# Kernel tuning notes

Hardware: AMD Instinct MI355X
Metric: run time of the kernel (lower is better)

## Reference

```python
import jax, jax.numpy as jnp
import numpy as np

D_MODEL = 1024
N_HEADS = 16
D_K = D_MODEL // N_HEADS


def setup_inputs() -> dict:
    key = jax.random.key(0)
    ks = jax.random.split(key, 7)
    B, S = 2, 2048
    q = jax.random.normal(ks[0], (B, S, D_MODEL), dtype=jnp.float32)
    k = jax.random.normal(ks[1], (B, S, D_MODEL), dtype=jnp.float32)
    v = jax.random.normal(ks[2], (B, S, D_MODEL), dtype=jnp.float32)
    mask = jnp.ones((B, 1, S, S), dtype=bool)
    scale = 1.0 / np.sqrt(D_MODEL)
    w_q = jax.random.normal(ks[3], (D_MODEL, D_MODEL), dtype=jnp.float32) * scale
    w_k = jax.random.normal(ks[4], (D_MODEL, D_MODEL), dtype=jnp.float32) * scale
    w_v = jax.random.normal(ks[5], (D_MODEL, D_MODEL), dtype=jnp.float32) * scale
    w_o = jax.random.normal(ks[6], (D_MODEL, D_MODEL), dtype=jnp.float32) * scale
    return {"q": q, "k": k, "v": v, "mask": mask,
            "w_q": w_q, "w_k": w_k, "w_v": w_v, "w_o": w_o}


def reference(q, k, v, mask, w_q, w_k, w_v, w_o):
    B, S, _ = q.shape
    # projections (nn.Linear: x @ W^T, no bias)
    def split_heads(x):  # [B,S,D] -> [B,H,S,d_k]
        return x.reshape(B, -1, N_HEADS, D_K).transpose(0, 2, 1, 3)
    query = split_heads(q @ w_q.T)
    key_h = split_heads(k @ w_k.T)
    value = split_heads(v @ w_v.T)
    # naive scaled dot-product attention: full [B,H,S,S] scores materialized
    scores = jnp.einsum('bhqd,bhkd->bhqk', query, key_h) / jnp.sqrt(
        jnp.asarray(D_K, query.dtype))
    scores = jnp.where(mask, scores, jnp.asarray(-1e9, scores.dtype))
    attn = jax.nn.softmax(scores, axis=-1)  # dropout p=0.0 -> identity
    x = jnp.einsum('bhqk,bhkd->bhqd', attn, value)
    x = x.transpose(0, 2, 1, 3).reshape(B, S, N_HEADS * D_K)
    return x @ w_o.T
```

## Files before the change

kernel.cpp:

```cpp
#include <hip/hip_runtime.h>
#include <hip/hip_bf16.h>
#include <math.h>

typedef __bf16 bf16;
typedef __bf16 bf16x8 __attribute__((ext_vector_type(8)));
typedef float f32x4 __attribute__((ext_vector_type(4)));

#define MFMA16(a, b, c) __builtin_amdgcn_mfma_f32_16x16x32_bf16((a), (b), (c), 0, 0, 0)

__device__ __forceinline__ void gl_lds16(const void* g, void* l) {
    __builtin_amdgcn_global_load_lds(
        (__attribute__((address_space(1))) void*)(g),
        (__attribute__((address_space(3))) void*)(l),
        16, 0, 0);
}

__global__ __launch_bounds__(256) void cvt7(
    const float* __restrict__ w0, const float* __restrict__ w1,
    const float* __restrict__ w2, const float* __restrict__ w3,
    const float* __restrict__ x0, const float* __restrict__ x1,
    const float* __restrict__ x2, bf16* __restrict__ dst) {
    const int z = blockIdx.y;
    const float* src;
    bf16* out;
    if (z < 4) {
        if (blockIdx.x >= 512) return;
        src = (z == 0) ? w0 : (z == 1) ? w1 : (z == 2) ? w2 : w3;
        out = dst + (size_t)z * 1048576;
    } else {
        src = (z == 4) ? x0 : (z == 5) ? x1 : x2;
        out = dst + 4 * 1048576 + (size_t)(z - 4) * 4194304;
    }
    const int i = (blockIdx.x * 256 + threadIdx.x) * 8;
    float4 a = ((const float4*)(src + i))[0];
    float4 b = ((const float4*)(src + i))[1];
    bf16x8 o;
    o[0] = (bf16)a.x; o[1] = (bf16)a.y; o[2] = (bf16)a.z; o[3] = (bf16)a.w;
    o[4] = (bf16)b.x; o[5] = (bf16)b.y; o[6] = (bf16)b.z; o[7] = (bf16)b.w;
    *(bf16x8*)(out + i) = o;
}

template <int EP>
__device__ __forceinline__ void gemm_bf(const bf16* __restrict__ A,
                                        const bf16* __restrict__ B,
                                        void* __restrict__ Cv,
                                        const int m0, const int n0) {
    constexpr int K = 1024;
    __shared__ __align__(16) bf16 As[128 * 32];
    __shared__ __align__(16) bf16 Bs[128 * 32];

    const int t = threadIdx.x;
    const int lane = t & 63;
    const int w = t >> 6;
    const int wm = (w & 1) * 64;
    const int wn = (w >> 1) * 64;
    const int lr = lane & 15;
    const int lq8 = (lane >> 4) * 8;
    const int rq = (lane >> 4) * 4;

    f32x4 acc[4][4] = {};

    const int srow = t >> 2;
    const int sch = (t & 3) * 8;
    char* lA = (char*)As;
    char* lB = (char*)Bs;

    for (int k0 = 0; k0 < K; k0 += 32) {
        gl_lds16(A + (size_t)(m0 + srow) * K + k0 + sch,      lA + t * 16);
        gl_lds16(A + (size_t)(m0 + 64 + srow) * K + k0 + sch, lA + 4096 + t * 16);
        gl_lds16(B + (size_t)(n0 + srow) * K + k0 + sch,      lB + t * 16);
        gl_lds16(B + (size_t)(n0 + 64 + srow) * K + k0 + sch, lB + 4096 + t * 16);
        __syncthreads();

        bf16x8 af[4], bfr[4];
#pragma unroll
        for (int i = 0; i < 4; ++i) {
            af[i]  = *(const bf16x8*)&As[(wm + i * 16 + lr) * 32 + lq8];
            bfr[i] = *(const bf16x8*)&Bs[(wn + i * 16 + lr) * 32 + lq8];
        }
#pragma unroll
        for (int mi = 0; mi < 4; ++mi)
#pragma unroll
            for (int ni = 0; ni < 4; ++ni)
                acc[mi][ni] = MFMA16(af[mi], bfr[ni], acc[mi][ni]);
        __syncthreads();
    }

#pragma unroll
    for (int mi = 0; mi < 4; ++mi) {
#pragma unroll
        for (int ni = 0; ni < 4; ++ni) {
#pragma unroll
            for (int r = 0; r < 4; ++r) {
                const int m = m0 + wm + mi * 16 + rq + r;
                const int n = n0 + wn + ni * 16 + lr;
                const float vv = acc[mi][ni][r];
                if constexpr (EP == 0) {
                    bf16* C = (bf16*)Cv;
                    const int b = m >> 11, s = m & 2047;
                    const int h = n >> 6,  d = n & 63;
                    C[(((size_t)(b * 16 + h)) * 2048 + s) * 64 + d] = (bf16)vv;
                } else if constexpr (EP == 1) {
                    float* C = (float*)Cv;
                    C[(size_t)m * 1024 + n] = vv;
                } else {
                    bf16* C = (bf16*)Cv;
                    C[((size_t)(n >> 11) * 1024 + m) * 2048 + (n & 2047)] = (bf16)vv;
                }
            }
        }
    }
}

__global__ __launch_bounds__(256, 3) void qkv_bf(
    const bf16* __restrict__ Xq, const bf16* __restrict__ Xk,
    const bf16* __restrict__ Xv, const bf16* __restrict__ Wc,
    bf16* __restrict__ Qb, bf16* __restrict__ Kb, bf16* __restrict__ Vb) {
    const int z = blockIdx.z;
    if (z == 0)
        gemm_bf<0>(Xq, Wc, Qb, blockIdx.x * 128, blockIdx.y * 128);
    else if (z == 1)
        gemm_bf<0>(Xk, Wc + 1048576, Kb, blockIdx.x * 128, blockIdx.y * 128);
    else
        gemm_bf<2>(Wc + 2 * 1048576, Xv, Vb, blockIdx.y * 128, blockIdx.x * 128);
}

__global__ __launch_bounds__(256, 2) void out_gemm(
    const bf16* __restrict__ X, const bf16* __restrict__ W, float* __restrict__ C) {
    gemm_bf<1>(X, W, C, blockIdx.x * 128, blockIdx.y * 128);
}

template <int MODE>
__device__ __forceinline__ void gemm_f32tok(const void* __restrict__ Av,
                                            const void* __restrict__ Bv,
                                            bf16* __restrict__ C,
                                            const int m0, const int n0) {
    constexpr int K = 1024;
    __shared__ __align__(16) bf16 As[128 * 32];
    __shared__ __align__(16) bf16 Bs[128 * 32];

    const int t = threadIdx.x;
    const int lane = t & 63;
    const int w = t >> 6;
    const int wm = (w & 1) * 64;
    const int wn = (w >> 1) * 64;
    const int lr = lane & 15;
    const int lq8 = (lane >> 4) * 8;
    const int rq = (lane >> 4) * 4;

    f32x4 acc[4][4] = {};
    const int srow = t >> 2;
    const int sch = (t & 3) * 8;
    const int ar = t >> 1;
    const int ac = (t & 1) * 16;
    char* lA = (char*)As;
    char* lB = (char*)Bs;

    for (int k0 = 0; k0 < K; k0 += 32) {
        if constexpr (MODE == 0) {
            const float* X = (const float*)Av;
            const float* p = X + (size_t)(m0 + ar) * K + k0 + ac;
            float4 f0 = ((const float4*)p)[0], f1 = ((const float4*)p)[1];
            float4 f2 = ((const float4*)p)[2], f3 = ((const float4*)p)[3];
            bf16x8 o0, o1;
            o0[0]=(bf16)f0.x; o0[1]=(bf16)f0.y; o0[2]=(bf16)f0.z; o0[3]=(bf16)f0.w;
            o0[4]=(bf16)f1.x; o0[5]=(bf16)f1.y; o0[6]=(bf16)f1.z; o0[7]=(bf16)f1.w;
            o1[0]=(bf16)f2.x; o1[1]=(bf16)f2.y; o1[2]=(bf16)f2.z; o1[3]=(bf16)f2.w;
            o1[4]=(bf16)f3.x; o1[5]=(bf16)f3.y; o1[6]=(bf16)f3.z; o1[7]=(bf16)f3.w;
            *(bf16x8*)&As[ar * 32 + ac]     = o0;
            *(bf16x8*)&As[ar * 32 + ac + 8] = o1;
        } else {
            const bf16* X = (const bf16*)Av;
            gl_lds16(X + (size_t)(m0 + srow) * K + k0 + sch,      lA + t * 16);
            gl_lds16(X + (size_t)(m0 + 64 + srow) * K + k0 + sch, lA + 4096 + t * 16);
        }
        if constexpr (MODE == 2) {
            const float* X = (const float*)Bv;
            const float* p = X + (size_t)(n0 + ar) * K + k0 + ac;
            float4 f0 = ((const float4*)p)[0], f1 = ((const float4*)p)[1];
            float4 f2 = ((const float4*)p)[2], f3 = ((const float4*)p)[3];
            bf16x8 o0, o1;
            o0[0]=(bf16)f0.x; o0[1]=(bf16)f0.y; o0[2]=(bf16)f0.z; o0[3]=(bf16)f0.w;
            o0[4]=(bf16)f1.x; o0[5]=(bf16)f1.y; o0[6]=(bf16)f1.z; o0[7]=(bf16)f1.w;
            o1[0]=(bf16)f2.x; o1[1]=(bf16)f2.y; o1[2]=(bf16)f2.z; o1[3]=(bf16)f2.w;
            o1[4]=(bf16)f3.x; o1[5]=(bf16)f3.y; o1[6]=(bf16)f3.z; o1[7]=(bf16)f3.w;
            *(bf16x8*)&Bs[ar * 32 + ac]     = o0;
            *(bf16x8*)&Bs[ar * 32 + ac + 8] = o1;
        } else {
            const bf16* W = (const bf16*)Bv;
            gl_lds16(W + (size_t)(n0 + srow) * K + k0 + sch,      lB + t * 16);
            gl_lds16(W + (size_t)(n0 + 64 + srow) * K + k0 + sch, lB + 4096 + t * 16);
        }
        __syncthreads();

        bf16x8 af[4], bfr[4];
#pragma unroll
        for (int i = 0; i < 4; ++i) {
            af[i]  = *(const bf16x8*)&As[(wm + i * 16 + lr) * 32 + lq8];
            bfr[i] = *(const bf16x8*)&Bs[(wn + i * 16 + lr) * 32 + lq8];
        }
#pragma unroll
        for (int mi = 0; mi < 4; ++mi)
#pragma unroll
            for (int ni = 0; ni < 4; ++ni)
                acc[mi][ni] = MFMA16(af[mi], bfr[ni], acc[mi][ni]);
        __syncthreads();
    }

#pragma unroll
    for (int mi = 0; mi < 4; ++mi) {
#pragma unroll
        for (int ni = 0; ni < 4; ++ni) {
#pragma unroll
            for (int r = 0; r < 4; ++r) {
                const int m = m0 + wm + mi * 16 + rq + r;
                const int n = n0 + wn + ni * 16 + lr;
                const float vv = acc[mi][ni][r];
                if constexpr (MODE == 0) {
                    const int b = m >> 11, s = m & 2047;
                    const int h = n >> 6,  d = n & 63;
                    C[(((size_t)(b * 16 + h)) * 2048 + s) * 64 + d] = (bf16)vv;
                } else {
                    C[((size_t)(n >> 11) * 1024 + m) * 2048 + (n & 2047)] = (bf16)vv;
                }
            }
        }
    }
}

__global__ __launch_bounds__(256, 2) void qkv_f32(
    const float* __restrict__ q, const float* __restrict__ k, const float* __restrict__ v,
    const bf16* __restrict__ Wc, bf16* __restrict__ Qb, bf16* __restrict__ Kb,
    bf16* __restrict__ Vb) {
    const int z = blockIdx.z;
    if (z == 0)
        gemm_f32tok<0>(q, Wc, Qb, blockIdx.x * 128, blockIdx.y * 128);
    else if (z == 1)
        gemm_f32tok<0>(k, Wc + 1048576, Kb, blockIdx.x * 128, blockIdx.y * 128);
    else
        gemm_f32tok<2>(Wc + 2 * 1048576, v, Vb, blockIdx.y * 128, blockIdx.x * 128);
}

__global__ __launch_bounds__(256, 4) void attn_kernel(
    const bf16* __restrict__ Qb, const bf16* __restrict__ Kb,
    const bf16* __restrict__ Vb, bf16* __restrict__ Xb) {
    constexpr int S = 2048;

    __shared__ __align__(16) bf16 Qs[64 * 64];
    __shared__ __align__(16) bf16 Ks[64 * 64];
    __shared__ __align__(16) bf16 Ps[64 * 64];
    __shared__ __align__(16) bf16 Vt[80 * 64];

    const int t = threadIdx.x;
    const int lane = t & 63;
    const int w = t >> 6;
    const int lr = lane & 15;
    const int lq8 = (lane >> 4) * 8;
    const int q4 = (lane >> 4) * 4;
    const int bh = blockIdx.y;
    const int q0 = blockIdx.x * 64;
    const bf16* Q  = Qb + (size_t)bh * S * 64;
    const bf16* Kh = Kb + (size_t)bh * S * 64;
    const bf16* Vh = Vb + (size_t)bh * 64 * S;

    const float qscale = 0.125f * 1.4426950408889634f;
#pragma unroll
    for (int p = 0; p < 2; ++p) {
        const int c = p * 256 + t;
        const int row = c >> 3, cc = c & 7;
        bf16x8 vq = *(const bf16x8*)(Q + (size_t)(q0 + row) * 64 + cc * 8);
#pragma unroll
        for (int e = 0; e < 8; ++e) vq[e] = (bf16)((float)vq[e] * qscale);
        *(bf16x8*)&Qs[row * 64 + (cc ^ (row & 7)) * 8] = vq;
    }
    for (int idx = t; idx < 1024; idx += 256) {
        const int r = idx >> 6;
        Vt[(64 + r) * 64 + (idx & 63)] = (r == 0) ? (bf16)1.0f : (bf16)0.0f;
    }

    f32x4 oacc[5] = {};

    const int srow = t >> 2;
    const int scc = (t & 3) * 2;
    bf16x8 pk[2], pv[2];
#pragma unroll
    for (int c = 0; c < 2; ++c) {
        pk[c] = *(const bf16x8*)(Kh + (size_t)srow * 64 + (scc + c) * 8);
        pv[c] = *(const bf16x8*)(Vh + (size_t)srow * S + (scc + c) * 8);
    }

    const int rowA = w * 16 + lr;
    const int swzA = (lr & 7) << 3;
    const int swzP = (((rowA >> 1) & 7)) << 3;

    for (int j = 0; j < S / 64; ++j) {
        __syncthreads();
#pragma unroll
        for (int c = 0; c < 2; ++c) {
            *(bf16x8*)&Ks[srow * 64 + ((scc + c) ^ (srow & 7)) * 8] = pk[c];
            *(bf16x8*)&Vt[srow * 64 + ((scc + c) ^ (srow & 7)) * 8] = pv[c];
        }
        __syncthreads();

        f32x4 sacc[4] = {};
#pragma unroll
        for (int ks = 0; ks < 64; ks += 32) {
            bf16x8 af = *(const bf16x8*)&Qs[rowA * 64 + ((ks + lq8) ^ swzA)];
            bf16x8 bk[4];
#pragma unroll
            for (int nt = 0; nt < 4; ++nt)
                bk[nt] = *(const bf16x8*)&Ks[(nt * 16 + lr) * 64 + ((ks + lq8) ^ swzA)];
#pragma unroll
            for (int nt = 0; nt < 4; ++nt)
                sacc[nt] = MFMA16(af, bk[nt], sacc[nt]);
        }

        if (j + 1 < S / 64) {
            const bf16* Kt = Kh + (size_t)(j + 1) * 64 * 64;
            const bf16* Vg = Vh + (size_t)(j + 1) * 64;
#pragma unroll
            for (int c = 0; c < 2; ++c) {
                pk[c] = *(const bf16x8*)(Kt + (size_t)srow * 64 + (scc + c) * 8);
                pv[c] = *(const bf16x8*)(Vg + (size_t)srow * S + (scc + c) * 8);
            }
        }

#pragma unroll
        for (int r = 0; r < 4; ++r) {
            const int row = w * 16 + q4 + r;
            const int swz = ((row >> 1) & 7) << 3;
#pragma unroll
            for (int nt = 0; nt < 4; ++nt)
                Ps[row * 64 + ((nt * 16 + lr) ^ swz)] =
                    (bf16)exp2f(fminf(sacc[nt][r], 100.f));
        }

#pragma unroll
        for (int ks = 0; ks < 64; ks += 32) {
            bf16x8 ap = *(const bf16x8*)&Ps[rowA * 64 + ((ks + lq8) ^ swzP)];
            bf16x8 bv[5];
#pragma unroll
            for (int nt2 = 0; nt2 < 5; ++nt2)
                bv[nt2] = *(const bf16x8*)&Vt[(nt2 * 16 + lr) * 64 + ((ks + lq8) ^ swzA)];
#pragma unroll
            for (int nt2 = 0; nt2 < 5; ++nt2)
                oacc[nt2] = MFMA16(ap, bv[nt2], oacc[nt2]);
        }
    }

    const int b = bh >> 4, h = bh & 15;
#pragma unroll
    for (int r = 0; r < 4; ++r) {
        const float lv = __shfl(oacc[4][r], lane & 48, 64);
        const float inv = 1.f / fmaxf(lv, 1e-30f);
        const int row = w * 16 + q4 + r;
        const size_t base = ((size_t)(b * 2048 + q0 + row)) * 1024 + h * 64;
#pragma unroll
        for (int nt2 = 0; nt2 < 4; ++nt2)
            Xb[base + nt2 * 16 + lr] = (bf16)(oacc[nt2][r] * inv);
    }
}

extern "C" void kernel_launch(void* const* d_in, const int* in_sizes, int n_in,
                              void* d_out, int out_size, void* d_ws, size_t ws_size,
                              hipStream_t stream) {
    const float* q  = (const float*)d_in[0];
    const float* k  = (const float*)d_in[1];
    const float* v  = (const float*)d_in[2];
    const float* wq = (const float*)d_in[4];
    const float* wk = (const float*)d_in[5];
    const float* wv = (const float*)d_in[6];
    const float* wo = (const float*)d_in[7];
    float* out = (float*)d_out;

    const bool big = ws_size >= (size_t)64 * 1024 * 1024;
    bf16* Wc = (bf16*)d_ws;
    const dim3 blk(256);

    if (big) {
        bf16* Xq = Wc + 4 * 1048576;
        bf16* Xk = Xq + 4194304;
        bf16* Xv = Xk + 4194304;
        bf16* Qb = Xv + 4194304;
        bf16* Kb = Qb + 4194304;
        bf16* Vb = Kb + 4194304;
        bf16* Xb = Vb + 4194304;
        cvt7<<<dim3(2048, 7), blk, 0, stream>>>(wq, wk, wv, wo, q, k, v, Wc);
        qkv_bf<<<dim3(32, 8, 3), blk, 0, stream>>>(Xq, Xk, Xv, Wc, Qb, Kb, Vb);
        attn_kernel<<<dim3(32, 32), blk, 0, stream>>>(Qb, Kb, Vb, Xb);
        out_gemm<<<dim3(32, 8), blk, 0, stream>>>(Xb, Wc + 3 * 1048576, out);
    } else {
        bf16* Qb = Wc + 4 * 1048576;
        bf16* Kb = Qb + 4194304;
        bf16* Vb = Kb + 4194304;
        bf16* Xb = Vb + 4194304;
        cvt7<<<dim3(512, 4), blk, 0, stream>>>(wq, wk, wv, wo, q, k, v, Wc);
        qkv_f32<<<dim3(32, 8, 3), blk, 0, stream>>>(q, k, v, Wc, Qb, Kb, Vb);
        attn_kernel<<<dim3(32, 32), blk, 0, stream>>>(Qb, Kb, Vb, Xb);
        out_gemm<<<dim3(32, 8), blk, 0, stream>>>(Xb, Wc + 3 * 1048576, out);
    }
}
```

Measured before the change: 262.7 us.

## Rewrite attention with 32x32 MFMA, register-resident P and 128-row query tiles

The attention kernel now uses 32x32x16 bf16 MFMAs. It computes S^T = K·Q^T so the exponentiated scores stay in registers and are repacked into the PV operand with cvt_pk_bf16 and permlane32_swap, which removes the Ps LDS round-trip and the Q LDS buffer. Each block now covers 128 query rows (32 per wave) instead of 64, halving K/V tile reloads per query. Row sums are accumulated in registers instead of through an extra ones-column MFMA. The trade-off is higher register pressure (launch bounds drop from 4 to 2) and half as many blocks.

```diff
diff --git a/kernel.cpp b/kernel.cpp
--- a/kernel.cpp
+++ b/kernel.cpp
@@ -5,14 +5,23 @@
 typedef __bf16 bf16;
 typedef __bf16 bf16x8 __attribute__((ext_vector_type(8)));
 typedef float f32x4 __attribute__((ext_vector_type(4)));
+typedef float f32x16 __attribute__((ext_vector_type(16)));
+typedef unsigned u32x4 __attribute__((ext_vector_type(4)));
 
 #define MFMA16(a, b, c) __builtin_amdgcn_mfma_f32_16x16x32_bf16((a), (b), (c), 0, 0, 0)
+#define MFMA32(a, b, c) __builtin_amdgcn_mfma_f32_32x32x16_bf16((a), (b), (c), 0, 0, 0)
 
 __device__ __forceinline__ void gl_lds16(const void* g, void* l) {
     __builtin_amdgcn_global_load_lds(
         (__attribute__((address_space(1))) void*)(g),
         (__attribute__((address_space(3))) void*)(l),
         16, 0, 0);
+}
+
+__device__ __forceinline__ unsigned cvt_pk_bf16(float lo, float hi) {
+    unsigned r;
+    asm("v_cvt_pk_bf16_f32 %0, %1, %2" : "=v"(r) : "v"(lo), "v"(hi));
+    return r;
 }
 
 __global__ __launch_bounds__(256) void cvt7(
@@ -241,44 +250,37 @@
         gemm_f32tok<2>(Wc + 2 * 1048576, v, Vb, blockIdx.y * 128, blockIdx.x * 128);
 }
 
-__global__ __launch_bounds__(256, 4) void attn_kernel(
+__global__ __launch_bounds__(256, 2) void attn_kernel(
     const bf16* __restrict__ Qb, const bf16* __restrict__ Kb,
     const bf16* __restrict__ Vb, bf16* __restrict__ Xb) {
     constexpr int S = 2048;
 
-    __shared__ __align__(16) bf16 Qs[64 * 64];
     __shared__ __align__(16) bf16 Ks[64 * 64];
-    __shared__ __align__(16) bf16 Ps[64 * 64];
-    __shared__ __align__(16) bf16 Vt[80 * 64];
+    __shared__ __align__(16) bf16 Vt[64 * 64];
 
     const int t = threadIdx.x;
     const int lane = t & 63;
     const int w = t >> 6;
-    const int lr = lane & 15;
-    const int lq8 = (lane >> 4) * 8;
-    const int q4 = (lane >> 4) * 4;
+    const int l31 = lane & 31;
+    const int half = lane >> 5;
     const int bh = blockIdx.y;
-    const int q0 = blockIdx.x * 64;
+    const int q0 = blockIdx.x * 128 + w * 32;
     const bf16* Q  = Qb + (size_t)bh * S * 64;
     const bf16* Kh = Kb + (size_t)bh * S * 64;
     const bf16* Vh = Vb + (size_t)bh * 64 * S;
 
     const float qscale = 0.125f * 1.4426950408889634f;
-#pragma unroll
-    for (int p = 0; p < 2; ++p) {
-        const int c = p * 256 + t;
-        const int row = c >> 3, cc = c & 7;
-        bf16x8 vq = *(const bf16x8*)(Q + (size_t)(q0 + row) * 64 + cc * 8);
-#pragma unroll
-        for (int e = 0; e < 8; ++e) vq[e] = (bf16)((float)vq[e] * qscale);
-        *(bf16x8*)&Qs[row * 64 + (cc ^ (row & 7)) * 8] = vq;
-    }
-    for (int idx = t; idx < 1024; idx += 256) {
-        const int r = idx >> 6;
-        Vt[(64 + r) * 64 + (idx & 63)] = (r == 0) ? (bf16)1.0f : (bf16)0.0f;
-    }
-
-    f32x4 oacc[5] = {};
+    bf16x8 qf[4];
+#pragma unroll
+    for (int c = 0; c < 4; ++c) {
+        bf16x8 v0 = *(const bf16x8*)(Q + (size_t)(q0 + l31) * 64 + c * 16 + half * 8);
+#pragma unroll
+        for (int e = 0; e < 8; ++e) v0[e] = (bf16)((float)v0[e] * qscale);
+        qf[c] = v0;
+    }
+
+    f32x16 od[2] = {};
+    float ls0 = 0.f, ls1 = 0.f, ls2 = 0.f, ls3 = 0.f;
 
     const int srow = t >> 2;
     const int scc = (t & 3) * 2;
@@ -289,10 +291,6 @@
         pv[c] = *(const bf16x8*)(Vh + (size_t)srow * S + (scc + c) * 8);
     }
 
-    const int rowA = w * 16 + lr;
-    const int swzA = (lr & 7) << 3;
-    const int swzP = (((rowA >> 1) & 7)) << 3;
-
     for (int j = 0; j < S / 64; ++j) {
         __syncthreads();
 #pragma unroll
@@ -302,17 +300,16 @@
         }
         __syncthreads();
 
-        f32x4 sacc[4] = {};
-#pragma unroll
-        for (int ks = 0; ks < 64; ks += 32) {
-            bf16x8 af = *(const bf16x8*)&Qs[rowA * 64 + ((ks + lq8) ^ swzA)];
-            bf16x8 bk[4];
-#pragma unroll
-            for (int nt = 0; nt < 4; ++nt)
-                bk[nt] = *(const bf16x8*)&Ks[(nt * 16 + lr) * 64 + ((ks + lq8) ^ swzA)];
-#pragma unroll
-            for (int nt = 0; nt < 4; ++nt)
-                sacc[nt] = MFMA16(af, bk[nt], sacc[nt]);
+        f32x16 sacc[2] = {};
+#pragma unroll
+        for (int kt = 0; kt < 2; ++kt) {
+            const int kr = kt * 32 + l31;
+            const int ksw = (kr & 7);
+#pragma unroll
+            for (int c = 0; c < 4; ++c) {
+                bf16x8 kf = *(const bf16x8*)&Ks[kr * 64 + ((c * 2 + half) ^ ksw) * 8];
+                sacc[kt] = MFMA32(kf, qf[c], sacc[kt]);
+            }
         }
 
         if (j + 1 < S / 64) {
@@ -326,38 +323,57 @@
         }
 
 #pragma unroll
-        for (int r = 0; r < 4; ++r) {
-            const int row = w * 16 + q4 + r;
-            const int swz = ((row >> 1) & 7) << 3;
-#pragma unroll
-            for (int nt = 0; nt < 4; ++nt)
-                Ps[row * 64 + ((nt * 16 + lr) ^ swz)] =
-                    (bf16)exp2f(fminf(sacc[nt][r], 100.f));
-        }
-
-#pragma unroll
-        for (int ks = 0; ks < 64; ks += 32) {
-            bf16x8 ap = *(const bf16x8*)&Ps[rowA * 64 + ((ks + lq8) ^ swzP)];
-            bf16x8 bv[5];
-#pragma unroll
-            for (int nt2 = 0; nt2 < 5; ++nt2)
-                bv[nt2] = *(const bf16x8*)&Vt[(nt2 * 16 + lr) * 64 + ((ks + lq8) ^ swzA)];
-#pragma unroll
-            for (int nt2 = 0; nt2 < 5; ++nt2)
-                oacc[nt2] = MFMA16(ap, bv[nt2], oacc[nt2]);
-        }
-    }
-
-    const int b = bh >> 4, h = bh & 15;
-#pragma unroll
-    for (int r = 0; r < 4; ++r) {
-        const float lv = __shfl(oacc[4][r], lane & 48, 64);
-        const float inv = 1.f / fmaxf(lv, 1e-30f);
-        const int row = w * 16 + q4 + r;
-        const size_t base = ((size_t)(b * 2048 + q0 + row)) * 1024 + h * 64;
-#pragma unroll
-        for (int nt2 = 0; nt2 < 4; ++nt2)
-            Xb[base + nt2 * 16 + lr] = (bf16)(oacc[nt2][r] * inv);
+        for (int kt = 0; kt < 2; ++kt) {
+            float ex[16];
+#pragma unroll
+            for (int r = 0; r < 16; ++r)
+                ex[r] = exp2f(fminf(sacc[kt][r], 100.f));
+            ls0 += ex[0] + ex[4] + ex[8]  + ex[12];
+            ls1 += ex[1] + ex[5] + ex[9]  + ex[13];
+            ls2 += ex[2] + ex[6] + ex[10] + ex[14];
+            ls3 += ex[3] + ex[7] + ex[11] + ex[15];
+
+            unsigned pa[8];
+#pragma unroll
+            for (int c2 = 0; c2 < 2; ++c2) {
+#pragma unroll
+                for (int wd = 0; wd < 2; ++wd) {
+                    unsigned x = cvt_pk_bf16(ex[c2 * 8 + wd * 2 + 0], ex[c2 * 8 + wd * 2 + 1]);
+                    unsigned y = cvt_pk_bf16(ex[c2 * 8 + wd * 2 + 4], ex[c2 * 8 + wd * 2 + 5]);
+                    asm("v_permlane32_swap_b32 %0, %1" : "+v"(x), "+v"(y));
+                    pa[c2 * 4 + wd]     = x;
+                    pa[c2 * 4 + wd + 2] = y;
+                }
+            }
+
+#pragma unroll
+            for (int c2 = 0; c2 < 2; ++c2) {
+                u32x4 aw;
+                aw[0] = pa[c2 * 4 + 0]; aw[1] = pa[c2 * 4 + 1];
+                aw[2] = pa[c2 * 4 + 2]; aw[3] = pa[c2 * 4 + 3];
+                bf16x8 ap = __builtin_bit_cast(bf16x8, aw);
+#pragma unroll
+                for (int dt = 0; dt < 2; ++dt) {
+                    const int vr = dt * 32 + l31;
+                    bf16x8 vf = *(const bf16x8*)
+                        &Vt[vr * 64 + (((kt * 4 + c2 * 2 + half) ^ (vr & 7))) * 8];
+                    od[dt] = MFMA32(ap, vf, od[dt]);
+                }
+            }
+        }
+    }
+
+    float lsum = ls0 + ls1 + ls2 + ls3;
+    const float ltot = lsum + __shfl_xor(lsum, 32);
+    const float inv = 1.f / fmaxf(ltot, 1e-30f);
+    const int b = bh >> 4, hh = bh & 15;
+#pragma unroll
+    for (int r = 0; r < 16; ++r) {
+        const int qrow = (r & 3) + 8 * (r >> 2) + 4 * half;
+        const float invr = __shfl(inv, qrow);
+        const size_t base = ((size_t)(b * 2048 + q0 + qrow)) * 1024 + hh * 64;
+        Xb[base + l31]      = (bf16)(od[0][r] * invr);
+        Xb[base + 32 + l31] = (bf16)(od[1][r] * invr);
     }
 }
 
@@ -387,7 +403,7 @@
         bf16* Xb = Vb + 4194304;
         cvt7<<<dim3(2048, 7), blk, 0, stream>>>(wq, wk, wv, wo, q, k, v, Wc);
         qkv_bf<<<dim3(32, 8, 3), blk, 0, stream>>>(Xq, Xk, Xv, Wc, Qb, Kb, Vb);
-        attn_kernel<<<dim3(32, 32), blk, 0, stream>>>(Qb, Kb, Vb, Xb);
+        attn_kernel<<<dim3(16, 32), blk, 0, stream>>>(Qb, Kb, Vb, Xb);
         out_gemm<<<dim3(32, 8), blk, 0, stream>>>(Xb, Wc + 3 * 1048576, out);
     } else {
         bf16* Qb = Wc + 4 * 1048576;
@@ -396,7 +412,7 @@
         bf16* Xb = Vb + 4194304;
         cvt7<<<dim3(512, 4), blk, 0, stream>>>(wq, wk, wv, wo, q, k, v, Wc);
         qkv_f32<<<dim3(32, 8, 3), blk, 0, stream>>>(q, k, v, Wc, Qb, Kb, Vb);
-        attn_kernel<<<dim3(32, 32), blk, 0, stream>>>(Qb, Kb, Vb, Xb);
+        attn_kernel<<<dim3(16, 32), blk, 0, stream>>>(Qb, Kb, Vb, Xb);
         out_gemm<<<dim3(32, 8), blk, 0, stream>>>(Xb, Wc + 3 * 1048576, out);
     }
 }
```

New measurement: 248.2 us. 1.06x faster.
